# Kernel optimization log

Hardware: AMD Instinct MI355X
Metric: run time of the kernel (lower is better)

The kernel has to match this reference:

```python
import jax, jax.numpy as jnp
import numpy as np

N_NODES = 200_000
N_EDGES = 12_800_000


def setup_inputs() -> dict:
    key = jax.random.key(0)
    k1, k2, k3, k4 = jax.random.split(key, 4)
    x = jax.random.normal(k1, (N_NODES, 2), dtype=jnp.float32)
    edge_index = jax.random.randint(k2, (2, N_EDGES), 0, N_NODES, dtype=jnp.int32)
    # Glorot-ish init for the two GCN linear layers
    W1 = jax.random.normal(k3, (2, 16), dtype=jnp.float32) * 0.5
    b1 = jnp.zeros((16,), dtype=jnp.float32)
    W2 = jax.random.normal(k4, (16, 2), dtype=jnp.float32) * 0.25
    b2 = jnp.zeros((2,), dtype=jnp.float32)
    return {"x": x, "W1": W1, "b1": b1, "W2": W2, "b2": b2, "edge_index": edge_index}


def gcn_conv(x, W, b, src, dst, num_nodes):
    # PyG GCNConv: add self-loops, deg from dst (col), norm = d_src^-1/2 * d_dst^-1/2,
    # out[i] = sum_{j->i} norm_e * (x_j W) + (1/deg_i) * (x_i W) + b
    h = x @ W  # [N, F_out]
    ones = jnp.ones(src.shape[0], dtype=h.dtype)
    deg = jax.ops.segment_sum(ones, dst, num_segments=num_nodes) + 1.0  # +1 self-loop
    dinv = jax.lax.rsqrt(deg)  # [N]
    norm = dinv[src] * dinv[dst]  # [E]
    agg = jax.ops.segment_sum(h[src] * norm[:, None], dst, num_segments=num_nodes)
    # self-loop contribution has norm dinv_i * dinv_i = 1/deg_i
    return agg + h * (1.0 / deg)[:, None] + b


def reference(x, W1, b1, W2, b2, edge_index):
    src, dst = edge_index[0], edge_index[1]
    h = gcn_conv(x, W1, b1, src, dst, N_NODES)
    h = jax.nn.relu(h)
    out = gcn_conv(h, W2, b2, src, dst, N_NODES)
    return out
```

## Files before the change

### kernel.cpp

```cpp
#include <hip/hip_runtime.h>


constexpr int N_NODES = 200000;
constexpr int N_EDGES = 12800000;
constexpr int RANGE_SHIFT = 8;
constexpr int K_BUCKETS = (N_NODES + 255) / 256;
constexpr int SORT_BLOCKS = 2048;
constexpr int CHUNK = N_EDGES / SORT_BLOCKS;
constexpr int SCAN_R = SORT_BLOCKS / 256;
constexpr int SEG = 4;

typedef unsigned uint32x4 __attribute__((ext_vector_type(4)));


__global__ __launch_bounds__(256) void hist_kernel(const int* __restrict__ dst,
                                                   unsigned* __restrict__ blockHist) {
    __shared__ unsigned h[K_BUCKETS];
    for (int i = threadIdx.x; i < K_BUCKETS; i += 256) h[i] = 0;
    __syncthreads();
    int base = blockIdx.x * CHUNK;
    for (int e = base + threadIdx.x; e < base + CHUNK; e += 256)
        atomicAdd(&h[((unsigned)dst[e]) >> RANGE_SHIFT], 1u);
    __syncthreads();
    unsigned* row = blockHist + (size_t)blockIdx.x * K_BUCKETS;
    for (int i = threadIdx.x; i < K_BUCKETS; i += 256) row[i] = h[i];
}

__global__ __launch_bounds__(256) void scan_perblock_kernel(unsigned* __restrict__ blockHist,
                                                            unsigned* __restrict__ bucketTotal) {
    int b = blockIdx.x, t = threadIdx.x;
    unsigned v[SCAN_R], run = 0;
#pragma unroll
    for (int j = 0; j < SCAN_R; j++) v[j] = blockHist[(size_t)(SCAN_R * t + j) * K_BUCKETS + b];
#pragma unroll
    for (int j = 0; j < SCAN_R; j++) { unsigned tmp = v[j]; v[j] = run; run += tmp; }
    __shared__ unsigned sh[256];
    sh[t] = run;
    __syncthreads();
    for (int off = 1; off < 256; off <<= 1) {
        unsigned add = (t >= off) ? sh[t - off] : 0u;
        __syncthreads();
        sh[t] += add;
        __syncthreads();
    }
    unsigned excl = sh[t] - run;
#pragma unroll
    for (int j = 0; j < SCAN_R; j++)
        blockHist[(size_t)(SCAN_R * t + j) * K_BUCKETS + b] = excl + v[j];
    if (t == 255) bucketTotal[b] = sh[255];
}

__global__ __launch_bounds__(1024) void scan_buckets_kernel(const unsigned* __restrict__ bucketTotal,
                                                            unsigned* __restrict__ bucketStart) {
    __shared__ unsigned sh[1024];
    int t = threadIdx.x;
    unsigned v = (t < K_BUCKETS) ? bucketTotal[t] : 0u;
    sh[t] = v;
    __syncthreads();
    for (int off = 1; off < 1024; off <<= 1) {
        unsigned add = (t >= off) ? sh[t - off] : 0u;
        __syncthreads();
        sh[t] += add;
        __syncthreads();
    }
    if (t < K_BUCKETS) bucketStart[t] = sh[t] - v;
    if (t == K_BUCKETS - 1) bucketStart[K_BUCKETS] = sh[t];
}

__global__ __launch_bounds__(256) void scatter_kernel(const int* __restrict__ src,
                                                      const int* __restrict__ dst,
                                                      const unsigned* __restrict__ blockHist,
                                                      const unsigned* __restrict__ bucketTotal,
                                                      const unsigned* __restrict__ bucketStart,
                                                      unsigned* __restrict__ sorted) {
    __shared__ unsigned s_cur[K_BUCKETS];
    __shared__ int      s_base[K_BUCKETS];
    __shared__ unsigned ssum[256];
    __shared__ unsigned ent[CHUNK];
    __shared__ unsigned short bk[CHUNK];

    int t = threadIdx.x;
    int k = blockIdx.x;
    int base = k * CHUNK;
    const unsigned* row  = blockHist + (size_t)k * K_BUCKETS;
    const unsigned* rowN = blockHist + (size_t)(k + 1) * K_BUCKETS;
    bool last = (k == SORT_BLOCKS - 1);

    unsigned v[4], g0[4], run = 0;
#pragma unroll
    for (int j = 0; j < 4; j++) {
        int idx = 4 * t + j;
        if (idx < K_BUCKETS) {
            unsigned r0 = row[idx];
            unsigned r1 = last ? bucketTotal[idx] : rowN[idx];
            g0[j] = r0;
            v[j]  = r1 - r0;
        } else { g0[j] = 0; v[j] = 0; }
    }
#pragma unroll
    for (int j = 0; j < 4; j++) { unsigned tmp = v[j]; v[j] = run; run += tmp; }
    ssum[t] = run;
    __syncthreads();
    for (int off = 1; off < 256; off <<= 1) {
        unsigned add = (t >= off) ? ssum[t - off] : 0u;
        __syncthreads();
        ssum[t] += add;
        __syncthreads();
    }
    unsigned excl = ssum[t] - run;
#pragma unroll
    for (int j = 0; j < 4; j++) {
        int idx = 4 * t + j;
        if (idx < K_BUCKETS) {
            unsigned st = excl + v[j];
            s_cur[idx]  = st;
            s_base[idx] = (int)(bucketStart[idx] + g0[j]) - (int)st;
        }
    }
    __syncthreads();

    for (int e = base + t; e < base + CHUNK; e += 256) {
        unsigned d = (unsigned)dst[e];
        unsigned s = (unsigned)src[e];
        unsigned b = d >> RANGE_SHIFT;
        unsigned lpos = atomicAdd(&s_cur[b], 1u);
        ent[lpos] = s | ((d & 255u) << 18);
        bk[lpos] = (unsigned short)b;
    }
    __syncthreads();

    for (int i = t; i < CHUNK; i += 256) {
        unsigned b = bk[i];
        sorted[s_base[b] + i] = ent[i];
    }
}


__device__ __forceinline__ void seg_bounds(const unsigned* __restrict__ bucketStart,
                                           int bid, int& e0, int& e1) {
    int b = bid >> 2, s = bid & 3;
    int s0 = bucketStart[b], len = bucketStart[b + 1] - s0;
    e0 = s0 + (len * s) / SEG;
    e1 = s0 + (len * (s + 1)) / SEG;
}

__global__ __launch_bounds__(256) void deg_part_kernel(const unsigned* __restrict__ sorted,
                                                       const unsigned* __restrict__ bucketStart,
                                                       unsigned* __restrict__ pcnt) {
    __shared__ unsigned cnt[256];
    int t = threadIdx.x;
    cnt[t] = 0;
    __syncthreads();
    int e0, e1;
    seg_bounds(bucketStart, blockIdx.x, e0, e1);

    int e0a = (e0 + 3) & ~3;
    if (e0a > e1) e0a = e1;
    if (t < e0a - e0) {
        unsigned w = sorted[e0 + t];
        atomicAdd(&cnt[(w >> 18) & 255u], 1u);
    }
    int nq = (e1 - e0a) >> 2;
    const uint32x4* q4 = (const uint32x4*)(sorted + e0a);
    int q = t;
    for (; q + 768 < nq; q += 1024) {
        uint32x4 w0 = q4[q];
        uint32x4 w1 = q4[q + 256];
        uint32x4 w2 = q4[q + 512];
        uint32x4 w3 = q4[q + 768];
#pragma unroll
        for (int j = 0; j < 4; j++) atomicAdd(&cnt[(w0[j] >> 18) & 255u], 1u);
#pragma unroll
        for (int j = 0; j < 4; j++) atomicAdd(&cnt[(w1[j] >> 18) & 255u], 1u);
#pragma unroll
        for (int j = 0; j < 4; j++) atomicAdd(&cnt[(w2[j] >> 18) & 255u], 1u);
#pragma unroll
        for (int j = 0; j < 4; j++) atomicAdd(&cnt[(w3[j] >> 18) & 255u], 1u);
    }
    for (; q < nq; q += 256) {
        uint32x4 w0 = q4[q];
#pragma unroll
        for (int j = 0; j < 4; j++) atomicAdd(&cnt[(w0[j] >> 18) & 255u], 1u);
    }
    int tail0 = e0a + (nq << 2);
    if (t < e1 - tail0) {
        unsigned w = sorted[tail0 + t];
        atomicAdd(&cnt[(w >> 18) & 255u], 1u);
    }
    __syncthreads();
    pcnt[(size_t)blockIdx.x * 256 + t] = cnt[t];
}

__global__ __launch_bounds__(256) void node1_kernel(const float2* __restrict__ x,
                                                    const unsigned* __restrict__ pcnt,
                                                    float* __restrict__ dinv,
                                                    float2* __restrict__ u) {
    int i = blockIdx.x * 256 + threadIdx.x;
    if (i >= N_NODES) return;
    int b = i >> 8, l = i & 255;
    unsigned c = 1;
#pragma unroll
    for (int s = 0; s < SEG; s++) c += pcnt[(size_t)(b * SEG + s) * 256 + l];
    float di = rsqrtf((float)c);
    dinv[i] = di;
    float2 xi = x[i];
    u[i] = make_float2(di * xi.x, di * xi.y);
}

__device__ __forceinline__ void agg_gather(const float2* __restrict__ table,
                                           const uint32x4 w, float2 v[4]) {
    v[0] = table[w[0] & 0x3FFFFu];
    v[1] = table[w[1] & 0x3FFFFu];
    v[2] = table[w[2] & 0x3FFFFu];
    v[3] = table[w[3] & 0x3FFFFu];
}

__device__ __forceinline__ void agg_accum(float* ax, float* ay,
                                          const uint32x4 w, const float2 v[4]) {
#pragma unroll
    for (int j = 0; j < 4; j++) {
        unsigned l = (w[j] >> 18) & 255u;
        atomicAdd(&ax[l], v[j].x);
        atomicAdd(&ay[l], v[j].y);
    }
}

__global__ __launch_bounds__(256) void agg_part_kernel(const unsigned* __restrict__ sorted,
                                                       const unsigned* __restrict__ bucketStart,
                                                       const float2* __restrict__ table,
                                                       float2* __restrict__ part) {
    __shared__ float ax[256], ay[256];
    int t = threadIdx.x;
    ax[t] = 0.f; ay[t] = 0.f;
    __syncthreads();
    int e0, e1;
    seg_bounds(bucketStart, blockIdx.x, e0, e1);

    int e0a = (e0 + 3) & ~3;
    if (e0a > e1) e0a = e1;
    if (t < e0a - e0) {
        unsigned w = sorted[e0 + t];
        float2 v = table[w & 0x3FFFFu];
        unsigned l = (w >> 18) & 255u;
        atomicAdd(&ax[l], v.x);
        atomicAdd(&ay[l], v.y);
    }
    int nq = (e1 - e0a) >> 2;
    const uint32x4* q4 = (const uint32x4*)(sorted + e0a);
    int q = t;
    for (; q + 768 < nq; q += 1024) {
        uint32x4 w0 = q4[q];
        uint32x4 w1 = q4[q + 256];
        uint32x4 w2 = q4[q + 512];
        uint32x4 w3 = q4[q + 768];
        float2 v0[4], v1[4], v2[4], v3[4];
        agg_gather(table, w0, v0);
        agg_gather(table, w1, v1);
        agg_gather(table, w2, v2);
        agg_gather(table, w3, v3);
        agg_accum(ax, ay, w0, v0);
        agg_accum(ax, ay, w1, v1);
        agg_accum(ax, ay, w2, v2);
        agg_accum(ax, ay, w3, v3);
    }
    for (; q < nq; q += 256) {
        uint32x4 w0 = q4[q];
        float2 v0[4];
        agg_gather(table, w0, v0);
        agg_accum(ax, ay, w0, v0);
    }
    int tail0 = e0a + (nq << 2);
    if (t < e1 - tail0) {
        unsigned w = sorted[tail0 + t];
        float2 v = table[w & 0x3FFFFu];
        unsigned l = (w >> 18) & 255u;
        atomicAdd(&ax[l], v.x);
        atomicAdd(&ay[l], v.y);
    }
    __syncthreads();
    part[(size_t)blockIdx.x * 256 + t] = make_float2(ax[t], ay[t]);
}

__global__ __launch_bounds__(256) void node2_kernel(const float2* __restrict__ u,
                                                    const float2* __restrict__ part,
                                                    const float* __restrict__ W1,
                                                    const float* __restrict__ b1,
                                                    const float* __restrict__ W2,
                                                    const float* __restrict__ dinv,
                                                    float2* __restrict__ g2) {
    int i = blockIdx.x * 256 + threadIdx.x;
    if (i >= N_NODES) return;
    int b = i >> 8, l = i & 255;
    float ax = 0.f, ay = 0.f;
#pragma unroll
    for (int s = 0; s < SEG; s++) {
        float2 p = part[(size_t)(b * SEG + s) * 256 + l];
        ax += p.x; ay += p.y;
    }
    float di = dinv[i];
    float2 uu = u[i];
    float c0 = di * (ax + uu.x);
    float c1 = di * (ay + uu.y);
    float a0 = 0.f, a1 = 0.f;
#pragma unroll
    for (int f = 0; f < 16; f++) {
        float o = fmaxf(c0 * W1[f] + c1 * W1[16 + f] + b1[f], 0.f);
        a0 += o * W2[2 * f];
        a1 += o * W2[2 * f + 1];
    }
    g2[i] = make_float2(di * a0, di * a1);
}

__global__ __launch_bounds__(256) void node3_kernel(const float2* __restrict__ g2,
                                                    const float2* __restrict__ part,
                                                    const float* __restrict__ b2,
                                                    const float* __restrict__ dinv,
                                                    float2* __restrict__ out) {
    int i = blockIdx.x * 256 + threadIdx.x;
    if (i >= N_NODES) return;
    int b = i >> 8, l = i & 255;
    float ax = 0.f, ay = 0.f;
#pragma unroll
    for (int s = 0; s < SEG; s++) {
        float2 p = part[(size_t)(b * SEG + s) * 256 + l];
        ax += p.x; ay += p.y;
    }
    float di = dinv[i];
    float2 g = g2[i];
    out[i] = make_float2(di * (ax + g.x) + b2[0],
                         di * (ay + g.y) + b2[1]);
}


__global__ __launch_bounds__(256) void fb_deg(const int* __restrict__ dst, int* __restrict__ degi) {
    int e = blockIdx.x * 256 + threadIdx.x;
    if (e < N_EDGES) atomicAdd(&degi[dst[e]], 1);
}
__global__ __launch_bounds__(256) void fb_node1(const float* __restrict__ x, const int* __restrict__ degi,
                                                float* __restrict__ dinv, float2* __restrict__ u) {
    int i = blockIdx.x * 256 + threadIdx.x;
    if (i >= N_NODES) return;
    float di = rsqrtf((float)(degi[i] + 1));
    dinv[i] = di;
    float2 xi = ((const float2*)x)[i];
    u[i] = make_float2(di * xi.x, di * xi.y);
}
__global__ __launch_bounds__(256) void fb_agg(const int* __restrict__ src, const int* __restrict__ dst,
                                              const float2* __restrict__ table, float* __restrict__ acc) {
    int e = blockIdx.x * 256 + threadIdx.x;
    if (e >= N_EDGES) return;
    float2 v = table[src[e]];
    size_t d = dst[e];
    unsafeAtomicAdd(&acc[2 * d], v.x);
    unsafeAtomicAdd(&acc[2 * d + 1], v.y);
}
__global__ __launch_bounds__(256) void fb_node2(const float2* __restrict__ u, const float2* __restrict__ A1,
                                                const float* __restrict__ W1, const float* __restrict__ b1,
                                                const float* __restrict__ W2, const float* __restrict__ dinv,
                                                float2* __restrict__ g2) {
    int i = blockIdx.x * 256 + threadIdx.x;
    if (i >= N_NODES) return;
    float di = dinv[i];
    float2 a = A1[i], uu = u[i];
    float c0 = di * (a.x + uu.x), c1 = di * (a.y + uu.y);
    float a0 = 0.f, a1 = 0.f;
#pragma unroll
    for (int f = 0; f < 16; f++) {
        float o = fmaxf(c0 * W1[f] + c1 * W1[16 + f] + b1[f], 0.f);
        a0 += o * W2[2 * f];
        a1 += o * W2[2 * f + 1];
    }
    g2[i] = make_float2(di * a0, di * a1);
}
__global__ __launch_bounds__(256) void fb_node3(const float2* __restrict__ g2, const float2* __restrict__ A2,
                                                const float* __restrict__ b2, const float* __restrict__ dinv,
                                                float2* __restrict__ out) {
    int i = blockIdx.x * 256 + threadIdx.x;
    if (i >= N_NODES) return;
    float di = dinv[i];
    float2 a = A2[i], g = g2[i];
    out[i] = make_float2(di * (a.x + g.x) + b2[0], di * (a.y + g.y) + b2[1]);
}


extern "C" void kernel_launch(void* const* d_in, const int* in_sizes, int n_in,
                              void* d_out, int out_size, void* d_ws, size_t ws_size,
                              hipStream_t stream) {
    const float* x  = (const float*)d_in[0];
    const float* W1 = (const float*)d_in[1];
    const float* b1 = (const float*)d_in[2];
    const float* W2 = (const float*)d_in[3];
    const float* b2 = (const float*)d_in[4];
    const int* ei   = (const int*)d_in[5];
    const int* src = ei;
    const int* dst = ei + N_EDGES;
    float2* out = (float2*)d_out;

    const size_t need = ((size_t)N_EDGES + (size_t)SORT_BLOCKS * K_BUCKETS + 782 + 784
                         + N_NODES + 2 * (size_t)N_NODES + 2 * (size_t)N_NODES) * 4;

    if (ws_size >= need) {
        unsigned* sorted      = (unsigned*)d_ws;
        unsigned* blockHist   = sorted + N_EDGES;
        unsigned* bucketTotal = blockHist + (size_t)SORT_BLOCKS * K_BUCKETS;
        unsigned* bucketStart = bucketTotal + 782;
        float*    dinv        = (float*)(bucketStart + 784);
        float2*   u           = (float2*)(dinv + N_NODES);
        float2*   g2          = u + N_NODES;
        unsigned* pcnt        = blockHist;
        float2*   part        = (float2*)blockHist;

        hist_kernel<<<SORT_BLOCKS, 256, 0, stream>>>(dst, blockHist);
        scan_perblock_kernel<<<K_BUCKETS, 256, 0, stream>>>(blockHist, bucketTotal);
        scan_buckets_kernel<<<1, 1024, 0, stream>>>(bucketTotal, bucketStart);
        scatter_kernel<<<SORT_BLOCKS, 256, 0, stream>>>(src, dst, blockHist, bucketTotal,
                                                        bucketStart, sorted);
        deg_part_kernel<<<K_BUCKETS * SEG, 256, 0, stream>>>(sorted, bucketStart, pcnt);
        node1_kernel<<<K_BUCKETS, 256, 0, stream>>>((const float2*)x, pcnt, dinv, u);
        agg_part_kernel<<<K_BUCKETS * SEG, 256, 0, stream>>>(sorted, bucketStart, u, part);
        node2_kernel<<<K_BUCKETS, 256, 0, stream>>>(u, part, W1, b1, W2, dinv, g2);
        agg_part_kernel<<<K_BUCKETS * SEG, 256, 0, stream>>>(sorted, bucketStart, g2, part);
        node3_kernel<<<K_BUCKETS, 256, 0, stream>>>(g2, part, b2, dinv, out);
    } else {
        float* ws = (float*)d_ws;
        int*   degi = (int*)ws;
        float* A1   = ws + N_NODES;
        float* A2   = A1 + 2 * (size_t)N_NODES;
        float* dinvF = A2 + 2 * (size_t)N_NODES;
        float2* uF  = (float2*)(dinvF + N_NODES);
        float2* g2F = uF + N_NODES;
        constexpr int EB = (N_EDGES + 255) / 256;
        constexpr int NB = (N_NODES + 255) / 256;
        (void)hipMemsetAsync(degi, 0, 5 * (size_t)N_NODES * sizeof(float), stream);
        fb_deg<<<EB, 256, 0, stream>>>(dst, degi);
        fb_node1<<<NB, 256, 0, stream>>>(x, degi, dinvF, uF);
        fb_agg<<<EB, 256, 0, stream>>>(src, dst, uF, A1);
        fb_node2<<<NB, 256, 0, stream>>>(uF, (const float2*)A1, W1, b1, W2, dinvF, g2F);
        fb_agg<<<EB, 256, 0, stream>>>(src, dst, g2F, A2);
        fb_node3<<<NB, 256, 0, stream>>>(g2F, (const float2*)A2, b2, dinvF, out);
    }
}
```

Baseline: 586.3 us.

## Sort edges into 2D dst-superblock × src-group bins for gather locality

```diff
diff --git a/kernel.cpp b/kernel.cpp
--- a/kernel.cpp
+++ b/kernel.cpp
@@ -3,38 +3,79 @@
 
 constexpr int N_NODES = 200000;
 constexpr int N_EDGES = 12800000;
-constexpr int RANGE_SHIFT = 8;
-constexpr int K_BUCKETS = (N_NODES + 255) / 256;
-constexpr int SORT_BLOCKS = 2048;
-constexpr int CHUNK = N_EDGES / SORT_BLOCKS;
-constexpr int SCAN_R = SORT_BLOCKS / 256;
-constexpr int SEG = 4;
+
+constexpr int SB_SHIFT = 12;
+constexpr int NSB = (N_NODES + 4095) / 4096;
+constexpr int SG_SHIFT = 11;
+constexpr int NSG = (N_NODES + 2047) / 2048;
+constexpr int NBIN = NSB * NSG;
+constexpr int S2B = 1024;
+constexpr int CH2 = N_EDGES / S2B;
+constexpr int R19 = 19;
+constexpr int DSEG = 24;
+constexpr int ASEG = 24;
 
 typedef unsigned uint32x4 __attribute__((ext_vector_type(4)));
 
 
-__global__ __launch_bounds__(256) void hist_kernel(const int* __restrict__ dst,
-                                                   unsigned* __restrict__ blockHist) {
-    __shared__ unsigned h[K_BUCKETS];
-    for (int i = threadIdx.x; i < K_BUCKETS; i += 256) h[i] = 0;
-    __syncthreads();
-    int base = blockIdx.x * CHUNK;
-    for (int e = base + threadIdx.x; e < base + CHUNK; e += 256)
-        atomicAdd(&h[((unsigned)dst[e]) >> RANGE_SHIFT], 1u);
-    __syncthreads();
-    unsigned* row = blockHist + (size_t)blockIdx.x * K_BUCKETS;
-    for (int i = threadIdx.x; i < K_BUCKETS; i += 256) row[i] = h[i];
-}
-
-__global__ __launch_bounds__(256) void scan_perblock_kernel(unsigned* __restrict__ blockHist,
-                                                            unsigned* __restrict__ bucketTotal) {
-    int b = blockIdx.x, t = threadIdx.x;
-    unsigned v[SCAN_R], run = 0;
-#pragma unroll
-    for (int j = 0; j < SCAN_R; j++) v[j] = blockHist[(size_t)(SCAN_R * t + j) * K_BUCKETS + b];
-#pragma unroll
-    for (int j = 0; j < SCAN_R; j++) { unsigned tmp = v[j]; v[j] = run; run += tmp; }
+__global__ __launch_bounds__(256) void hist2_kernel(const int* __restrict__ src,
+                                                    const int* __restrict__ dst,
+                                                    unsigned short* __restrict__ bh16) {
+    __shared__ unsigned h[NBIN];
+    int t = threadIdx.x;
+    for (int i = t; i < NBIN; i += 256) h[i] = 0;
+    __syncthreads();
+    int base = blockIdx.x * CH2;
+    for (int e = base + t; e < base + CH2; e += 256) {
+        unsigned d = (unsigned)dst[e];
+        unsigned s = (unsigned)src[e];
+        atomicAdd(&h[(d >> SB_SHIFT) * NSG + (s >> SG_SHIFT)], 1u);
+    }
+    __syncthreads();
+    unsigned short* row = bh16 + (size_t)blockIdx.x * NBIN;
+    for (int i = t; i < NBIN; i += 256) row[i] = (unsigned short)h[i];
+}
+
+__global__ __launch_bounds__(256) void scan2_kernel(unsigned short* __restrict__ bh16,
+                                                    unsigned* __restrict__ binTotal) {
+    __shared__ unsigned psum[16][17];
+    int t = threadIdx.x;
+    int binL = t & 15, chunk = t >> 4;
+    int bin = blockIdx.x * 16 + binL;
+    bool ok = bin < NBIN;
+    unsigned s = 0;
+    if (ok) {
+        for (int r = chunk * 64; r < chunk * 64 + 64; ++r)
+            s += bh16[(size_t)r * NBIN + bin];
+    }
+    psum[chunk][binL] = s;
+    __syncthreads();
+    if (chunk == 0 && ok) {
+        unsigned run = 0;
+        for (int c = 0; c < 16; ++c) { unsigned tmp = psum[c][binL]; psum[c][binL] = run; run += tmp; }
+        binTotal[bin] = run;
+    }
+    __syncthreads();
+    if (ok) {
+        unsigned run = psum[chunk][binL];
+        for (int r = chunk * 64; r < chunk * 64 + 64; ++r) {
+            size_t idx = (size_t)r * NBIN + bin;
+            unsigned tmp = bh16[idx];
+            bh16[idx] = (unsigned short)run;
+            run += tmp;
+        }
+    }
+}
+
+__global__ __launch_bounds__(256) void scan_bins2_kernel(const unsigned* __restrict__ binTotal,
+                                                         unsigned* __restrict__ binStart) {
     __shared__ unsigned sh[256];
+    int t = threadIdx.x;
+    unsigned v[R19], run = 0;
+#pragma unroll
+    for (int j = 0; j < R19; j++) { int idx = R19 * t + j; v[j] = (idx < NBIN) ? binTotal[idx] : 0u; }
+#pragma unroll
+    for (int j = 0; j < R19; j++) { unsigned tmp = v[j]; v[j] = run; run += tmp; }
     sh[t] = run;
     __syncthreads();
     for (int off = 1; off < 256; off <<= 1) {
@@ -45,60 +86,41 @@
     }
     unsigned excl = sh[t] - run;
 #pragma unroll
-    for (int j = 0; j < SCAN_R; j++)
-        blockHist[(size_t)(SCAN_R * t + j) * K_BUCKETS + b] = excl + v[j];
-    if (t == 255) bucketTotal[b] = sh[255];
-}
-
-__global__ __launch_bounds__(1024) void scan_buckets_kernel(const unsigned* __restrict__ bucketTotal,
-                                                            unsigned* __restrict__ bucketStart) {
-    __shared__ unsigned sh[1024];
-    int t = threadIdx.x;
-    unsigned v = (t < K_BUCKETS) ? bucketTotal[t] : 0u;
-    sh[t] = v;
-    __syncthreads();
-    for (int off = 1; off < 1024; off <<= 1) {
-        unsigned add = (t >= off) ? sh[t - off] : 0u;
-        __syncthreads();
-        sh[t] += add;
-        __syncthreads();
-    }
-    if (t < K_BUCKETS) bucketStart[t] = sh[t] - v;
-    if (t == K_BUCKETS - 1) bucketStart[K_BUCKETS] = sh[t];
-}
-
-__global__ __launch_bounds__(256) void scatter_kernel(const int* __restrict__ src,
-                                                      const int* __restrict__ dst,
-                                                      const unsigned* __restrict__ blockHist,
-                                                      const unsigned* __restrict__ bucketTotal,
-                                                      const unsigned* __restrict__ bucketStart,
-                                                      unsigned* __restrict__ sorted) {
-    __shared__ unsigned s_cur[K_BUCKETS];
-    __shared__ int      s_base[K_BUCKETS];
+    for (int j = 0; j < R19; j++) { int idx = R19 * t + j; if (idx < NBIN) binStart[idx] = excl + v[j]; }
+    if (t == 255) binStart[NBIN] = sh[255];
+}
+
+__global__ __launch_bounds__(256) void scatter2_kernel(const int* __restrict__ src,
+                                                       const int* __restrict__ dst,
+                                                       const unsigned short* __restrict__ bh16,
+                                                       const unsigned* __restrict__ binTotal,
+                                                       const unsigned* __restrict__ binStart,
+                                                       unsigned* __restrict__ sorted) {
+    __shared__ unsigned s_cur[NBIN];
     __shared__ unsigned ssum[256];
-    __shared__ unsigned ent[CHUNK];
-    __shared__ unsigned short bk[CHUNK];
+    __shared__ unsigned ent[CH2];
+    __shared__ unsigned short bkk[CH2];
 
     int t = threadIdx.x;
     int k = blockIdx.x;
-    int base = k * CHUNK;
-    const unsigned* row  = blockHist + (size_t)k * K_BUCKETS;
-    const unsigned* rowN = blockHist + (size_t)(k + 1) * K_BUCKETS;
-    bool last = (k == SORT_BLOCKS - 1);
-
-    unsigned v[4], g0[4], run = 0;
-#pragma unroll
-    for (int j = 0; j < 4; j++) {
-        int idx = 4 * t + j;
-        if (idx < K_BUCKETS) {
+    int base = k * CH2;
+    const unsigned short* row  = bh16 + (size_t)k * NBIN;
+    const unsigned short* rowN = bh16 + (size_t)(k + 1) * NBIN;
+    bool last = (k == S2B - 1);
+
+    unsigned v[R19], g0[R19], run = 0;
+#pragma unroll
+    for (int j = 0; j < R19; j++) {
+        int idx = R19 * t + j;
+        if (idx < NBIN) {
             unsigned r0 = row[idx];
-            unsigned r1 = last ? bucketTotal[idx] : rowN[idx];
+            unsigned r1 = last ? binTotal[idx] : (unsigned)rowN[idx];
             g0[j] = r0;
             v[j]  = r1 - r0;
         } else { g0[j] = 0; v[j] = 0; }
     }
 #pragma unroll
-    for (int j = 0; j < 4; j++) { unsigned tmp = v[j]; v[j] = run; run += tmp; }
+    for (int j = 0; j < R19; j++) { unsigned tmp = v[j]; v[j] = run; run += tmp; }
     ssum[t] = run;
     __syncthreads();
     for (int off = 1; off < 256; off <<= 1) {
@@ -109,56 +131,62 @@
     }
     unsigned excl = ssum[t] - run;
 #pragma unroll
-    for (int j = 0; j < 4; j++) {
-        int idx = 4 * t + j;
-        if (idx < K_BUCKETS) {
-            unsigned st = excl + v[j];
-            s_cur[idx]  = st;
-            s_base[idx] = (int)(bucketStart[idx] + g0[j]) - (int)st;
-        }
-    }
-    __syncthreads();
-
-    for (int e = base + t; e < base + CHUNK; e += 256) {
+    for (int j = 0; j < R19; j++) {
+        int idx = R19 * t + j;
+        if (idx < NBIN) s_cur[idx] = excl + v[j];
+    }
+    __syncthreads();
+
+    for (int e = base + t; e < base + CH2; e += 256) {
         unsigned d = (unsigned)dst[e];
         unsigned s = (unsigned)src[e];
-        unsigned b = d >> RANGE_SHIFT;
+        unsigned b = (d >> SB_SHIFT) * NSG + (s >> SG_SHIFT);
         unsigned lpos = atomicAdd(&s_cur[b], 1u);
-        ent[lpos] = s | ((d & 255u) << 18);
-        bk[lpos] = (unsigned short)b;
-    }
-    __syncthreads();
-
-    for (int i = t; i < CHUNK; i += 256) {
-        unsigned b = bk[i];
-        sorted[s_base[b] + i] = ent[i];
-    }
-}
-
-
-__device__ __forceinline__ void seg_bounds(const unsigned* __restrict__ bucketStart,
-                                           int bid, int& e0, int& e1) {
-    int b = bid >> 2, s = bid & 3;
-    int s0 = bucketStart[b], len = bucketStart[b + 1] - s0;
-    e0 = s0 + (len * s) / SEG;
-    e1 = s0 + (len * (s + 1)) / SEG;
-}
-
-__global__ __launch_bounds__(256) void deg_part_kernel(const unsigned* __restrict__ sorted,
-                                                       const unsigned* __restrict__ bucketStart,
-                                                       unsigned* __restrict__ pcnt) {
-    __shared__ unsigned cnt[256];
-    int t = threadIdx.x;
-    cnt[t] = 0;
-    __syncthreads();
-    int e0, e1;
-    seg_bounds(bucketStart, blockIdx.x, e0, e1);
+        ent[lpos] = s | ((d & 4095u) << 18);
+        bkk[lpos] = (unsigned short)b;
+    }
+    __syncthreads();
+
+#pragma unroll
+    for (int j = 0; j < R19; j++) {
+        int idx = R19 * t + j;
+        if (idx < NBIN) {
+            unsigned st = excl + v[j];
+            s_cur[idx] = (unsigned)((int)(binStart[idx] + g0[j]) - (int)st);
+        }
+    }
+    __syncthreads();
+
+    for (int i = t; i < CH2; i += 256) {
+        unsigned b = bkk[i];
+        sorted[(int)s_cur[b] + i] = ent[i];
+    }
+}
+
+
+__global__ __launch_bounds__(256) void zero_kernel(unsigned* __restrict__ p, int n) {
+    int i = blockIdx.x * 256 + threadIdx.x;
+    if (i < n) p[i] = 0u;
+}
+
+__global__ __launch_bounds__(256) void deg2_kernel(const unsigned* __restrict__ sorted,
+                                                   const unsigned* __restrict__ binStart,
+                                                   unsigned* __restrict__ deg) {
+    __shared__ unsigned cnt[4096];
+    int t = threadIdx.x;
+    for (int i = t; i < 4096; i += 256) cnt[i] = 0;
+    __syncthreads();
+    int sb = blockIdx.x / DSEG, s = blockIdx.x % DSEG;
+    int s0 = binStart[sb * NSG];
+    int len = binStart[(sb + 1) * NSG] - s0;
+    int e0 = s0 + (len * s) / DSEG;
+    int e1 = s0 + (len * (s + 1)) / DSEG;
 
     int e0a = (e0 + 3) & ~3;
     if (e0a > e1) e0a = e1;
     if (t < e0a - e0) {
         unsigned w = sorted[e0 + t];
-        atomicAdd(&cnt[(w >> 18) & 255u], 1u);
+        atomicAdd(&cnt[(w >> 18) & 4095u], 1u);
     }
     int nq = (e1 - e0a) >> 2;
     const uint32x4* q4 = (const uint32x4*)(sorted + e0a);
@@ -169,40 +197,40 @@
         uint32x4 w2 = q4[q + 512];
         uint32x4 w3 = q4[q + 768];
 #pragma unroll
-        for (int j = 0; j < 4; j++) atomicAdd(&cnt[(w0[j] >> 18) & 255u], 1u);
-#pragma unroll
-        for (int j = 0; j < 4; j++) atomicAdd(&cnt[(w1[j] >> 18) & 255u], 1u);
-#pragma unroll
-        for (int j = 0; j < 4; j++) atomicAdd(&cnt[(w2[j] >> 18) & 255u], 1u);
-#pragma unroll
-        for (int j = 0; j < 4; j++) atomicAdd(&cnt[(w3[j] >> 18) & 255u], 1u);
+        for (int j = 0; j < 4; j++) atomicAdd(&cnt[(w0[j] >> 18) & 4095u], 1u);
+#pragma unroll
+        for (int j = 0; j < 4; j++) atomicAdd(&cnt[(w1[j] >> 18) & 4095u], 1u);
+#pragma unroll
+        for (int j = 0; j < 4; j++) atomicAdd(&cnt[(w2[j] >> 18) & 4095u], 1u);
+#pragma unroll
+        for (int j = 0; j < 4; j++) atomicAdd(&cnt[(w3[j] >> 18) & 4095u], 1u);
     }
     for (; q < nq; q += 256) {
         uint32x4 w0 = q4[q];
 #pragma unroll
-        for (int j = 0; j < 4; j++) atomicAdd(&cnt[(w0[j] >> 18) & 255u], 1u);
+        for (int j = 0; j < 4; j++) atomicAdd(&cnt[(w0[j] >> 18) & 4095u], 1u);
     }
     int tail0 = e0a + (nq << 2);
     if (t < e1 - tail0) {
         unsigned w = sorted[tail0 + t];
-        atomicAdd(&cnt[(w >> 18) & 255u], 1u);
-    }
-    __syncthreads();
-    pcnt[(size_t)blockIdx.x * 256 + t] = cnt[t];
-}
-
-__global__ __launch_bounds__(256) void node1_kernel(const float2* __restrict__ x,
-                                                    const unsigned* __restrict__ pcnt,
-                                                    float* __restrict__ dinv,
-                                                    float2* __restrict__ u) {
-    int i = blockIdx.x * 256 + threadIdx.x;
-    if (i >= N_NODES) return;
-    int b = i >> 8, l = i & 255;
-    unsigned c = 1;
-#pragma unroll
-    for (int s = 0; s < SEG; s++) c += pcnt[(size_t)(b * SEG + s) * 256 + l];
+        atomicAdd(&cnt[(w >> 18) & 4095u], 1u);
+    }
+    __syncthreads();
+    int nb = sb << SB_SHIFT;
+    for (int i = t; i < 4096; i += 256) {
+        int node = nb + i;
+        if (node < N_NODES && cnt[i]) atomicAdd(&deg[node], cnt[i]);
+    }
+}
+
+__global__ __launch_bounds__(256) void node1n_kernel(const float2* __restrict__ x,
+                                                     unsigned* __restrict__ degdinv,
+                                                     float2* __restrict__ u) {
+    int i = blockIdx.x * 256 + threadIdx.x;
+    if (i >= N_NODES) return;
+    unsigned c = degdinv[i] + 1u;
     float di = rsqrtf((float)c);
-    dinv[i] = di;
+    ((float*)degdinv)[i] = di;
     float2 xi = x[i];
     u[i] = make_float2(di * xi.x, di * xi.y);
 }
@@ -219,29 +247,32 @@
                                           const uint32x4 w, const float2 v[4]) {
 #pragma unroll
     for (int j = 0; j < 4; j++) {
-        unsigned l = (w[j] >> 18) & 255u;
+        unsigned l = (w[j] >> 18) & 4095u;
         atomicAdd(&ax[l], v[j].x);
         atomicAdd(&ay[l], v[j].y);
     }
 }
 
-__global__ __launch_bounds__(256) void agg_part_kernel(const unsigned* __restrict__ sorted,
-                                                       const unsigned* __restrict__ bucketStart,
-                                                       const float2* __restrict__ table,
-                                                       float2* __restrict__ part) {
-    __shared__ float ax[256], ay[256];
-    int t = threadIdx.x;
-    ax[t] = 0.f; ay[t] = 0.f;
-    __syncthreads();
-    int e0, e1;
-    seg_bounds(bucketStart, blockIdx.x, e0, e1);
+__global__ __launch_bounds__(256) void agg2_kernel(const unsigned* __restrict__ sorted,
+                                                   const unsigned* __restrict__ binStart,
+                                                   const float2* __restrict__ table,
+                                                   float* __restrict__ acc) {
+    __shared__ float ax[4096], ay[4096];
+    int t = threadIdx.x;
+    for (int i = t; i < 4096; i += 256) { ax[i] = 0.f; ay[i] = 0.f; }
+    __syncthreads();
+    int sb = blockIdx.x / ASEG, s = blockIdx.x % ASEG;
+    int s0 = binStart[sb * NSG];
+    int len = binStart[(sb + 1) * NSG] - s0;
+    int e0 = s0 + (len * s) / ASEG;
+    int e1 = s0 + (len * (s + 1)) / ASEG;
 
     int e0a = (e0 + 3) & ~3;
     if (e0a > e1) e0a = e1;
     if (t < e0a - e0) {
         unsigned w = sorted[e0 + t];
         float2 v = table[w & 0x3FFFFu];
-        unsigned l = (w >> 18) & 255u;
+        unsigned l = (w >> 18) & 4095u;
         atomicAdd(&ax[l], v.x);
         atomicAdd(&ay[l], v.y);
     }
@@ -273,34 +304,33 @@
     if (t < e1 - tail0) {
         unsigned w = sorted[tail0 + t];
         float2 v = table[w & 0x3FFFFu];
-        unsigned l = (w >> 18) & 255u;
+        unsigned l = (w >> 18) & 4095u;
         atomicAdd(&ax[l], v.x);
         atomicAdd(&ay[l], v.y);
     }
     __syncthreads();
-    part[(size_t)blockIdx.x * 256 + t] = make_float2(ax[t], ay[t]);
-}
-
-__global__ __launch_bounds__(256) void node2_kernel(const float2* __restrict__ u,
-                                                    const float2* __restrict__ part,
-                                                    const float* __restrict__ W1,
-                                                    const float* __restrict__ b1,
-                                                    const float* __restrict__ W2,
-                                                    const float* __restrict__ dinv,
-                                                    float2* __restrict__ g2) {
-    int i = blockIdx.x * 256 + threadIdx.x;
-    if (i >= N_NODES) return;
-    int b = i >> 8, l = i & 255;
-    float ax = 0.f, ay = 0.f;
-#pragma unroll
-    for (int s = 0; s < SEG; s++) {
-        float2 p = part[(size_t)(b * SEG + s) * 256 + l];
-        ax += p.x; ay += p.y;
-    }
+    int nb = sb << SB_SHIFT;
+    for (int i = t; i < 4096; i += 256) {
+        int node = nb + i;
+        if (node < N_NODES) {
+            unsafeAtomicAdd(&acc[2 * node],     ax[i]);
+            unsafeAtomicAdd(&acc[2 * node + 1], ay[i]);
+        }
+    }
+}
+
+__global__ __launch_bounds__(256) void node2n_kernel(const float2* __restrict__ acc,
+                                                     float2* __restrict__ u,
+                                                     const float* __restrict__ W1,
+                                                     const float* __restrict__ b1,
+                                                     const float* __restrict__ W2,
+                                                     const float* __restrict__ dinv) {
+    int i = blockIdx.x * 256 + threadIdx.x;
+    if (i >= N_NODES) return;
     float di = dinv[i];
-    float2 uu = u[i];
-    float c0 = di * (ax + uu.x);
-    float c1 = di * (ay + uu.y);
+    float2 a = acc[i], uu = u[i];
+    float c0 = di * (a.x + uu.x);
+    float c1 = di * (a.y + uu.y);
     float a0 = 0.f, a1 = 0.f;
 #pragma unroll
     for (int f = 0; f < 16; f++) {
@@ -308,27 +338,20 @@
         a0 += o * W2[2 * f];
         a1 += o * W2[2 * f + 1];
     }
-    g2[i] = make_float2(di * a0, di * a1);
-}
-
-__global__ __launch_bounds__(256) void node3_kernel(const float2* __restrict__ g2,
-                                                    const float2* __restrict__ part,
-                                                    const float* __restrict__ b2,
-                                                    const float* __restrict__ dinv,
-                                                    float2* __restrict__ out) {
-    int i = blockIdx.x * 256 + threadIdx.x;
-    if (i >= N_NODES) return;
-    int b = i >> 8, l = i & 255;
-    float ax = 0.f, ay = 0.f;
-#pragma unroll
-    for (int s = 0; s < SEG; s++) {
-        float2 p = part[(size_t)(b * SEG + s) * 256 + l];
-        ax += p.x; ay += p.y;
-    }
+    u[i] = make_float2(di * a0, di * a1);
+}
+
+__global__ __launch_bounds__(256) void node3n_kernel(const float2* __restrict__ acc,
+                                                     const float2* __restrict__ g2,
+                                                     const float* __restrict__ b2,
+                                                     const float* __restrict__ dinv,
+                                                     float2* __restrict__ out) {
+    int i = blockIdx.x * 256 + threadIdx.x;
+    if (i >= N_NODES) return;
     float di = dinv[i];
-    float2 g = g2[i];
-    out[i] = make_float2(di * (ax + g.x) + b2[0],
-                         di * (ay + g.y) + b2[1]);
+    float2 a = acc[i], g = g2[i];
+    out[i] = make_float2(di * (a.x + g.x) + b2[0],
+                         di * (a.y + g.y) + b2[1]);
 }
 
 
@@ -396,31 +419,30 @@
     const int* dst = ei + N_EDGES;
     float2* out = (float2*)d_out;
 
-    const size_t need = ((size_t)N_EDGES + (size_t)SORT_BLOCKS * K_BUCKETS + 782 + 784
-                         + N_NODES + 2 * (size_t)N_NODES + 2 * (size_t)N_NODES) * 4;
+    const size_t need = ((size_t)N_EDGES + (size_t)S2B * NBIN / 2 + NBIN + 4806) * 4;
 
     if (ws_size >= need) {
-        unsigned* sorted      = (unsigned*)d_ws;
-        unsigned* blockHist   = sorted + N_EDGES;
-        unsigned* bucketTotal = blockHist + (size_t)SORT_BLOCKS * K_BUCKETS;
-        unsigned* bucketStart = bucketTotal + 782;
-        float*    dinv        = (float*)(bucketStart + 784);
-        float2*   u           = (float2*)(dinv + N_NODES);
-        float2*   g2          = u + N_NODES;
-        unsigned* pcnt        = blockHist;
-        float2*   part        = (float2*)blockHist;
-
-        hist_kernel<<<SORT_BLOCKS, 256, 0, stream>>>(dst, blockHist);
-        scan_perblock_kernel<<<K_BUCKETS, 256, 0, stream>>>(blockHist, bucketTotal);
-        scan_buckets_kernel<<<1, 1024, 0, stream>>>(bucketTotal, bucketStart);
-        scatter_kernel<<<SORT_BLOCKS, 256, 0, stream>>>(src, dst, blockHist, bucketTotal,
-                                                        bucketStart, sorted);
-        deg_part_kernel<<<K_BUCKETS * SEG, 256, 0, stream>>>(sorted, bucketStart, pcnt);
-        node1_kernel<<<K_BUCKETS, 256, 0, stream>>>((const float2*)x, pcnt, dinv, u);
-        agg_part_kernel<<<K_BUCKETS * SEG, 256, 0, stream>>>(sorted, bucketStart, u, part);
-        node2_kernel<<<K_BUCKETS, 256, 0, stream>>>(u, part, W1, b1, W2, dinv, g2);
-        agg_part_kernel<<<K_BUCKETS * SEG, 256, 0, stream>>>(sorted, bucketStart, g2, part);
-        node3_kernel<<<K_BUCKETS, 256, 0, stream>>>(g2, part, b2, dinv, out);
+        unsigned* sorted        = (unsigned*)d_ws;
+        unsigned short* bh16    = (unsigned short*)(sorted + N_EDGES);
+        unsigned* deg           = (unsigned*)bh16;
+        float*    dinv          = (float*)deg;
+        float*    acc           = (float*)(deg + N_NODES);
+        float2*   u             = (float2*)(acc + 2 * (size_t)N_NODES);
+        unsigned* binTotal      = (unsigned*)(bh16 + (size_t)S2B * NBIN);
+        unsigned* binStart      = binTotal + NBIN;
+
+        hist2_kernel<<<S2B, 256, 0, stream>>>(src, dst, bh16);
+        scan2_kernel<<<(NBIN + 15) / 16, 256, 0, stream>>>(bh16, binTotal);
+        scan_bins2_kernel<<<1, 256, 0, stream>>>(binTotal, binStart);
+        scatter2_kernel<<<S2B, 256, 0, stream>>>(src, dst, bh16, binTotal, binStart, sorted);
+        zero_kernel<<<(600000 + 255) / 256, 256, 0, stream>>>(deg, 600000);
+        deg2_kernel<<<NSB * DSEG, 256, 0, stream>>>(sorted, binStart, deg);
+        node1n_kernel<<<(N_NODES + 255) / 256, 256, 0, stream>>>((const float2*)x, deg, u);
+        agg2_kernel<<<NSB * ASEG, 256, 0, stream>>>(sorted, binStart, u, acc);
+        node2n_kernel<<<(N_NODES + 255) / 256, 256, 0, stream>>>((const float2*)acc, u, W1, b1, W2, dinv);
+        zero_kernel<<<(400000 + 255) / 256, 256, 0, stream>>>((unsigned*)acc, 400000);
+        agg2_kernel<<<NSB * ASEG, 256, 0, stream>>>(sorted, binStart, u, acc);
+        node3n_kernel<<<(N_NODES + 255) / 256, 256, 0, stream>>>((const float2*)acc, u, b2, dinv, out);
     } else {
         float* ws = (float*)d_ws;
         int*   degi = (int*)ws;
```

New measurement: 699.3 us. 1.19x slower.
